# Kernel tuning notes

Hardware: AMD Instinct MI355X
Metric: run time of the kernel (lower is better)

The kernel has to match this reference:

```python
import jax, jax.numpy as jnp
import numpy as np

N = 50000      # num nodes
E = 800000     # num edges (avg degree 16)
H = 128        # hidden_dim
D = 3          # node_dim (decoder output)
L = 4          # num_layers


def setup_inputs() -> dict:
    key = jax.random.key(0)
    ks = jax.random.split(key, 6)
    s = 0.05
    x = jax.random.normal(ks[0], (N, H), dtype=jnp.float32)
    edge_index = jax.random.randint(ks[1], (2, E), 0, N, dtype=jnp.int64)
    # per-layer EdgeConv MLP params: Linear(2H->H), ReLU, Linear(H->H)
    W1 = jax.random.normal(ks[2], (L, 2 * H, H), dtype=jnp.float32) * s
    b1 = jnp.zeros((L, H), dtype=jnp.float32)
    W2 = jax.random.normal(ks[3], (L, H, H), dtype=jnp.float32) * s
    b2 = jnp.zeros((L, H), dtype=jnp.float32)
    # final fc: Linear(H -> D)
    Wf = jax.random.normal(ks[4], (H, D), dtype=jnp.float32) * s
    bf = jnp.zeros((D,), dtype=jnp.float32)
    return {"x": x, "edge_index": edge_index, "W1": W1, "b1": b1,
            "W2": W2, "b2": b2, "Wf": Wf, "bf": bf}


def reference(x, edge_index, W1, b1, W2, b2, Wf, bf):
    n = x.shape[0]
    # add_self_loops: every node has at least one incoming message
    loops = jnp.arange(n, dtype=edge_index.dtype)
    src = jnp.concatenate([edge_index[0], loops])  # x_j source
    dst = jnp.concatenate([edge_index[1], loops])  # x_i target / aggregate index
    for l in range(W1.shape[0]):
        x_i = x[dst]                                   # [E+N, H] gather targets
        x_j = x[src]                                   # [E+N, H] gather sources
        msg = jnp.concatenate([x_i, x_j - x_i], axis=-1)   # [E+N, 2H]
        msg = jax.nn.relu(msg @ W1[l] + b1[l]) @ W2[l] + b2[l]  # edge MLP
        x = jax.ops.segment_max(msg, dst, num_segments=n)       # max aggregate
    return x @ Wf + bf  # [N, D]
```

## Files before the change

kernel.cpp:

```cpp
#include <hip/hip_runtime.h>
#include <hip/hip_fp16.h>

typedef _Float16 f16;
typedef _Float16 f16x8 __attribute__((ext_vector_type(8)));
typedef __fp16 hf16x2 __attribute__((ext_vector_type(2)));
typedef float f32x4 __attribute__((ext_vector_type(4)));
typedef float f32x2 __attribute__((ext_vector_type(2)));
typedef unsigned int u32;
typedef u32 u32x4 __attribute__((ext_vector_type(4)));

#define HDIM 128
#define LAYERS 4
#define TS 32
#define NEG_BIG (-3.0e38f)

static __device__ __forceinline__ f32x4 mfma16(f16x8 a, f16x8 b, f32x4 c) {
  return __builtin_amdgcn_mfma_f32_16x16x32_f16(a, b, c, 0, 0, 0);
}

static __device__ __forceinline__ void atomicMaxF(float* addr, float val) {
  if (val >= 0.f) atomicMax((int*)addr, __float_as_int(val));
  else            atomicMin((unsigned int*)addr, __float_as_uint(val));
}

static __device__ __forceinline__ f16x8 pack4(hf16x2 a, hf16x2 b, hf16x2 c, hf16x2 d) {
  u32x4 u = {__builtin_bit_cast(u32, a), __builtin_bit_cast(u32, b),
             __builtin_bit_cast(u32, c), __builtin_bit_cast(u32, d)};
  return __builtin_bit_cast(f16x8, u);
}

static __device__ __forceinline__ void split8(f32x4 a, f32x4 b, f16x8& hv, f16x8& lv) {
  hf16x2 h0 = __builtin_amdgcn_cvt_pkrtz(a.x, a.y);
  hf16x2 h1 = __builtin_amdgcn_cvt_pkrtz(a.z, a.w);
  hf16x2 h2 = __builtin_amdgcn_cvt_pkrtz(b.x, b.y);
  hf16x2 h3 = __builtin_amdgcn_cvt_pkrtz(b.z, b.w);
  hv = pack4(h0, h1, h2, h3);
  hf16x2 l0 = __builtin_amdgcn_cvt_pkrtz(a.x - (float)h0[0], a.y - (float)h0[1]);
  hf16x2 l1 = __builtin_amdgcn_cvt_pkrtz(a.z - (float)h1[0], a.w - (float)h1[1]);
  hf16x2 l2 = __builtin_amdgcn_cvt_pkrtz(b.x - (float)h2[0], b.y - (float)h2[1]);
  hf16x2 l3 = __builtin_amdgcn_cvt_pkrtz(b.z - (float)h3[0], b.w - (float)h3[1]);
  lv = pack4(l0, l1, l2, l3);
}

__global__ void gnn_hist(const int* __restrict__ ei, int* __restrict__ deg, int E) {
  int e = blockIdx.x * 256 + threadIdx.x;
  if (e < E) atomicAdd(&deg[ei[E + e]], 1);
}

__global__ void gnn_bsum(const int* __restrict__ deg, int* __restrict__ bsum, int N) {
  __shared__ int red[256];
  int v = blockIdx.x * 256 + threadIdx.x;
  red[threadIdx.x] = (v < N) ? (deg[v] + 1) : 0;
  __syncthreads();
  for (int d = 128; d; d >>= 1) {
    if (threadIdx.x < d) red[threadIdx.x] += red[threadIdx.x + d];
    __syncthreads();
  }
  if (threadIdx.x == 0) bsum[blockIdx.x] = red[0];
}

__global__ void gnn_bscan(const int* __restrict__ bsum, int* __restrict__ boffs,
                          int* __restrict__ offs, int nb, int N) {
  __shared__ int sh[256];
  int t = threadIdx.x;
  sh[t] = (t < nb) ? bsum[t] : 0;
  __syncthreads();
  for (int d = 1; d < 256; d <<= 1) {
    int add = (t >= d) ? sh[t - d] : 0;
    __syncthreads();
    sh[t] += add;
    __syncthreads();
  }
  boffs[t] = (t > 0) ? sh[t - 1] : 0;
  if (t == 255) offs[N] = sh[255];
}

__global__ void gnn_scan_fin(const int* __restrict__ deg, const int* __restrict__ boffs,
                             int* __restrict__ offs, int* __restrict__ cursor,
                             int* __restrict__ colsrc, int* __restrict__ nodeof, int N) {
  __shared__ int sh[256];
  int t = threadIdx.x;
  int v = blockIdx.x * 256 + t;
  int val = (v < N) ? (deg[v] + 1) : 0;
  sh[t] = val;
  __syncthreads();
  for (int d = 1; d < 256; d <<= 1) {
    int add = (t >= d) ? sh[t - d] : 0;
    __syncthreads();
    sh[t] += add;
    __syncthreads();
  }
  if (v < N) {
    int excl = boffs[blockIdx.x] + sh[t] - val;
    offs[v] = excl;
    cursor[v] = excl + 1;
    colsrc[excl] = v;
    nodeof[excl] = v;
  }
}

__global__ void gnn_scatter(const int* __restrict__ ei, int* __restrict__ cursor,
                            int* __restrict__ colsrc, int* __restrict__ nodeof, int E) {
  int e = blockIdx.x * 256 + threadIdx.x;
  if (e < E) {
    int d = ei[E + e];
    int p = atomicAdd(&cursor[d], 1);
    colsrc[p] = ei[e];
    nodeof[p] = d;
  }
}

__global__ void gnn_biasprep(const float* __restrict__ W1, const float* __restrict__ b1,
                             const float* __restrict__ b2, const float* __restrict__ Wf,
                             const float* __restrict__ bf, float* __restrict__ cbias,
                             float* __restrict__ bfp) {
  int l = blockIdx.x, c = threadIdx.x;
  if (l < LAYERS) {
    float s = 0.f;
    if (l > 0) {
      const float* bp = b2 + (size_t)(l - 1) * HDIM;
      if (c < 128) {
        for (int k = 0; k < 128; k++)
          s += bp[k] * (W1[((size_t)l * 256 + k) * 128 + c] - W1[((size_t)l * 256 + 128 + k) * 128 + c]);
      } else {
        int cc = c - 128;
        for (int k = 0; k < 128; k++)
          s += bp[k] * W1[((size_t)l * 256 + 128 + k) * 128 + cc];
      }
    }
    float base = (c < 128) ? b1[(size_t)l * HDIM + c] : 0.f;
    cbias[l * 256 + c] = base + s;
  } else if (c < 3) {
    float s = bf[c];
    for (int k = 0; k < 128; k++) s += b2[3 * HDIM + k] * Wf[k * 3 + c];
    bfp[c] = s;
  }
}

__global__ void gnn_wprep1(const float* __restrict__ W1, f16* __restrict__ Wc) {
  int id = blockIdx.x * 256 + threadIdx.x;
  if (id >= LAYERS * 128 * 256) return;
  int col = id & 255, k = (id >> 8) & 127, l = id >> 15;
  float w;
  if (col < 128) w = W1[((size_t)l * 256 + k) * 128 + col] - W1[((size_t)l * 256 + 128 + k) * 128 + col];
  else           w = W1[((size_t)l * 256 + 128 + k) * 128 + (col - 128)];
  f16 hi = (f16)w;
  f16 lo = (f16)(w - (float)hi);
  int kk = k >> 5, quad = (k >> 3) & 3, j = k & 7;
  int ntile = col >> 4, lane = quad * 16 + (col & 15);
  size_t base = ((((size_t)l * 2 + 0) * 4 + kk) * 16 + ntile) * 512 + lane * 8 + j;
  Wc[base] = hi;
  Wc[base + (size_t)4 * 16 * 512] = lo;
}

__global__ void gnn_wprep2(const float* __restrict__ W2, f16* __restrict__ W2f) {
  int id = blockIdx.x * 256 + threadIdx.x;
  if (id >= LAYERS * 128 * 128) return;
  int n = id & 127, k = (id >> 7) & 127, l = id >> 14;
  float w = W2[((size_t)l * 128 + k) * 128 + n];
  f16 hi = (f16)w;
  f16 lo = (f16)(w - (float)hi);
  int kk = k >> 5, quad = (k >> 3) & 3, j = k & 7;
  int ntile = n >> 4, lane = quad * 16 + (n & 15);
  size_t base = ((((size_t)l * 2 + 0) * 4 + kk) * 8 + ntile) * 512 + lane * 8 + j;
  W2f[base] = hi;
  W2f[base + (size_t)4 * 8 * 512] = lo;
}

__global__ __launch_bounds__(256) void gnn_pq(const float* __restrict__ x,
    const f16* __restrict__ Wc, const float* __restrict__ cbias,
    float* __restrict__ P, float* __restrict__ Q, int N,
    const int* __restrict__ offs, int spb, float* __restrict__ xinit) {
  __shared__ __align__(16) f16 shA[2 * 4 * 4 * 64 * 8];
  int tid = threadIdx.x;
  int row0 = blockIdx.x * 64;
#pragma unroll
  for (int i = 0; i < 4; i++) {
    int p = i * 256 + tid;
    int row = p & 63, seg = p >> 6;
    f32x4 a = {}, b = {};
    int gr = row0 + row;
    if (gr < N) {
      const f32x4* xp = (const f32x4*)(x + (size_t)gr * HDIM + seg * 8);
      a = xp[0]; b = xp[1];
    }
    f16x8 hv, lv;
    split8(a, b, hv, lv);
    int kk = seg >> 2, quad = seg & 3, mt = row >> 4, m = row & 15;
    int lane = quad * 16 + m;
    int off = ((kk * 4 + mt) * 64 + lane) * 8;
    *(f16x8*)&shA[off] = hv;
    *(f16x8*)&shA[off + 4 * 4 * 64 * 8] = lv;
  }
  __syncthreads();
  int wave = tid >> 6, lane = tid & 63;
  int quad = lane >> 4, cl = lane & 15;
  f16x8 bw[2][4][4];
#pragma unroll
  for (int pl = 0; pl < 2; pl++)
#pragma unroll
    for (int nt = 0; nt < 4; nt++)
#pragma unroll
      for (int kk = 0; kk < 4; kk++) {
        int ntile = wave * 4 + nt;
        bw[pl][nt][kk] = *(const f16x8*)&Wc[(((size_t)(pl * 4 + kk) * 16 + ntile) * 64 + lane) * 8];
      }
#pragma unroll
  for (int mt = 0; mt < 4; mt++) {
    f32x4 acc[4] = {};
#pragma unroll
    for (int kk = 0; kk < 4; kk++) {
      f16x8 ah = *(const f16x8*)&shA[((kk * 4 + mt) * 64 + lane) * 8];
      f16x8 al = *(const f16x8*)&shA[(((4 + kk) * 4 + mt) * 64 + lane) * 8];
#pragma unroll
      for (int nt = 0; nt < 4; nt++) {
        acc[nt] = mfma16(ah, bw[0][nt][kk], acc[nt]);
        acc[nt] = mfma16(al, bw[0][nt][kk], acc[nt]);
        acc[nt] = mfma16(ah, bw[1][nt][kk], acc[nt]);
      }
    }
#pragma unroll
    for (int nt = 0; nt < 4; nt++) {
      int c = (wave * 4 + nt) * 16 + cl;
      float bb = cbias[c];
      float* dst = (c < HDIM) ? P : Q;
      int cc = c & 127;
#pragma unroll
      for (int i = 0; i < 4; i++) {
        int gr = row0 + mt * 16 + quad * 4 + i;
        if (gr < N) dst[(size_t)gr * HDIM + cc] = acc[nt][i] + bb;
      }
    }
  }
  if (tid < 64) {
    int v = row0 + tid;
    if (v < N) {
      int a = offs[v], b = offs[v + 1] - 1;
      if (a / spb != b / spb) {
        f32x4 ninf = {NEG_BIG, NEG_BIG, NEG_BIG, NEG_BIG};
        float* xr = xinit + (size_t)v * HDIM;
#pragma unroll
        for (int c = 0; c < HDIM; c += 4) *(f32x4*)(xr + c) = ninf;
      }
    }
  }
}

__global__ __launch_bounds__(256, 4) void gnn_edge8(
    const float* __restrict__ P, const float* __restrict__ Q,
    const int* __restrict__ offs, const int* __restrict__ colsrc,
    const int* __restrict__ nodeof, const f16* __restrict__ W2f,
    float* __restrict__ xout, int S, int spb) {
  __shared__ __align__(16) f16 shA[2 * 4 * 2 * 64 * 8];
  __shared__ __align__(16) float stradV[2][128];
  __shared__ int stradN[2];
  int tid = threadIdx.x;
  int wave = tid >> 6, lane = tid & 63;
  int quad = lane >> 4, cl = lane & 15;
  f16x8 bw[2][2][4];
#pragma unroll
  for (int pl = 0; pl < 2; pl++)
#pragma unroll
    for (int nt = 0; nt < 2; nt++)
#pragma unroll
      for (int kk = 0; kk < 4; kk++)
        bw[pl][nt][kk] = *(const f16x8*)&W2f[(((size_t)(pl * 4 + kk) * 8 + (wave * 2 + nt)) * 64 + lane) * 8];
  int blk0 = blockIdx.x * spb;
  int blk1 = blk0 + spb; if (blk1 > S) blk1 = S;
  if (tid < 2) stradN[tid] = -1;
  __syncthreads();
  int sl = tid >> 4, seg = tid & 15;
  int kkb = seg >> 2, qb = seg & 3;
  int laneF = qb * 16 + sl;
  int Sm1 = S - 1;
  int tc = 0;
  for (int t0 = blk0; t0 < blk1; t0 += TS, tc++) {
    int par = tc & 1, prv = par ^ 1;
    int tEnd = t0 + TS; if (tEnd > blk1) tEnd = blk1;
#pragma unroll
    for (int i = 0; i < 2; i++) {
      int slot = t0 + i * 16 + sl;
      int slc = (slot < S) ? slot : Sm1;
      int src = colsrc[slc];
      int dst = nodeof[slc];
      const f32x4* qp = (const f32x4*)(Q + (size_t)src * HDIM + seg * 8);
      const f32x4* pp = (const f32x4*)(P + (size_t)dst * HDIM + seg * 8);
      f32x4 qa = qp[0], qb4 = qp[1], pa = pp[0], pb = pp[1];
      f32x4 sa, sb;
      sa.x = fmaxf(pa.x + qa.x, 0.f); sa.y = fmaxf(pa.y + qa.y, 0.f);
      sa.z = fmaxf(pa.z + qa.z, 0.f); sa.w = fmaxf(pa.w + qa.w, 0.f);
      sb.x = fmaxf(pb.x + qb4.x, 0.f); sb.y = fmaxf(pb.y + qb4.y, 0.f);
      sb.z = fmaxf(pb.z + qb4.z, 0.f); sb.w = fmaxf(pb.w + qb4.w, 0.f);
      f16x8 hv, lv;
      split8(sa, sb, hv, lv);
      int off = ((kkb * 2 + i) * 64 + laneF) * 8;
      *(f16x8*)&shA[off] = hv;
      *(f16x8*)&shA[off + 4096] = lv;
    }
    __syncthreads();
    f32x4 acc[2][2] = {};
#pragma unroll
    for (int kk = 0; kk < 4; kk++)
#pragma unroll
      for (int mt = 0; mt < 2; mt++) {
        int off = ((kk * 2 + mt) * 64 + lane) * 8;
        f16x8 ah = *(const f16x8*)&shA[off];
        f16x8 al = *(const f16x8*)&shA[off + 4096];
#pragma unroll
        for (int nt = 0; nt < 2; nt++) {
          acc[mt][nt] = mfma16(ah, bw[0][nt][kk], acc[mt][nt]);
          acc[mt][nt] = mfma16(al, bw[0][nt][kk], acc[mt][nt]);
          acc[mt][nt] = mfma16(ah, bw[1][nt][kk], acc[mt][nt]);
        }
      }
    __syncthreads();
    int vA = nodeof[t0];
    int vB = nodeof[tEnd - 1];
    int sNp = stradN[prv];
    for (int v = vA; v <= vB; v++) {
      int a = offs[v], b = offs[v + 1];
      int r0 = (a > t0 ? a : t0) - t0;
      int r1 = (b < tEnd ? b : tEnd) - t0;
      float m0 = NEG_BIG, m1 = NEG_BIG;
#pragma unroll
      for (int mt = 0; mt < 2; mt++)
#pragma unroll
        for (int i = 0; i < 4; i++) {
          int row = mt * 16 + quad * 4 + i;
          bool in = (row >= r0) && (row < r1);
          m0 = fmaxf(m0, in ? acc[mt][0][i] : NEG_BIG);
          m1 = fmaxf(m1, in ? acc[mt][1][i] : NEG_BIG);
        }
      m0 = fmaxf(m0, __shfl_xor(m0, 16, 64));
      m0 = fmaxf(m0, __shfl_xor(m0, 32, 64));
      m1 = fmaxf(m1, __shfl_xor(m1, 16, 64));
      m1 = fmaxf(m1, __shfl_xor(m1, 32, 64));
      if (quad == 0) {
        int col0 = wave * 32 + cl, col1 = col0 + 16;
        if (v == sNp) {
          m0 = fmaxf(m0, stradV[prv][col0]);
          m1 = fmaxf(m1, stradV[prv][col1]);
        }
        bool carry = (b > tEnd) && (tEnd < blk1);
        if (carry) {
          stradV[par][col0] = m0;
          stradV[par][col1] = m1;
        } else {
          float* dp = &xout[(size_t)v * HDIM];
          if (a < blk0 || b > blk1) {
            atomicMaxF(dp + col0, m0);
            atomicMaxF(dp + col1, m1);
          } else {
            dp[col0] = m0;
            dp[col1] = m1;
          }
        }
        if (wave == 0 && cl == 0 && v == vB) stradN[par] = carry ? v : -1;
      }
    }
  }
}

__global__ __launch_bounds__(256) void gnn_fc(const float* __restrict__ x,
    const float* __restrict__ Wf, const float* __restrict__ bfp,
    float* __restrict__ out, int N) {
  int wave = threadIdx.x >> 6, lane = threadIdx.x & 63;
  int wid = blockIdx.x * 4 + wave, nw = gridDim.x * 4;
  int k0 = lane * 2;
  float w00 = Wf[k0 * 3 + 0], w01 = Wf[k0 * 3 + 1], w02 = Wf[k0 * 3 + 2];
  float w10 = Wf[k0 * 3 + 3], w11 = Wf[k0 * 3 + 4], w12 = Wf[k0 * 3 + 5];
  float bf0 = bfp[0], bf1 = bfp[1], bf2 = bfp[2];
  for (int v = wid; v < N; v += nw) {
    f32x2 xx = *(const f32x2*)(x + (size_t)v * HDIM + k0);
    float d0 = xx.x * w00 + xx.y * w10;
    float d1 = xx.x * w01 + xx.y * w11;
    float d2 = xx.x * w02 + xx.y * w12;
#pragma unroll
    for (int s = 32; s; s >>= 1) {
      d0 += __shfl_xor(d0, s, 64);
      d1 += __shfl_xor(d1, s, 64);
      d2 += __shfl_xor(d2, s, 64);
    }
    if (lane == 0) {
      out[(size_t)v * 3 + 0] = d0 + bf0;
      out[(size_t)v * 3 + 1] = d1 + bf1;
      out[(size_t)v * 3 + 2] = d2 + bf2;
    }
  }
}

extern "C" void kernel_launch(void* const* d_in, const int* in_sizes, int n_in,
                              void* d_out, int out_size, void* d_ws, size_t ws_size,
                              hipStream_t stream) {
  const float* x_in = (const float*)d_in[0];
  const int*   ei   = (const int*)d_in[1];
  const float* W1   = (const float*)d_in[2];
  const float* b1   = (const float*)d_in[3];
  const float* W2   = (const float*)d_in[4];
  const float* b2   = (const float*)d_in[5];
  const float* Wf   = (const float*)d_in[6];
  const float* bfv  = (const float*)d_in[7];
  float* outp = (float*)d_out;
  int N = in_sizes[0] / HDIM;
  int E = in_sizes[1] / 2;
  int S = E + N;

  char* ws = (char*)d_ws;
  size_t o = 0;
  auto alloc = [&](size_t bytes) -> char* {
    char* p = ws + o;
    o += (bytes + 255) & ~(size_t)255;
    return p;
  };
  int*   deg    = (int*)alloc((size_t)N * 4);
  int*   offs   = (int*)alloc(((size_t)N + 1) * 4);
  int*   cursor = (int*)alloc((size_t)N * 4);
  int*   colsrc = (int*)alloc((size_t)S * 4);
  int*   nodeof = (int*)alloc((size_t)S * 4);
  int*   bsum   = (int*)alloc(256 * 4);
  int*   boffs  = (int*)alloc(256 * 4);
  float* cbias  = (float*)alloc((size_t)LAYERS * 256 * 4);
  float* bfp    = (float*)alloc(4 * 4);
  float* P      = (float*)alloc((size_t)N * HDIM * 4);
  float* Q      = (float*)alloc((size_t)N * HDIM * 4);
  float* xbuf   = (float*)alloc((size_t)N * HDIM * 4);
  f16*   Wc     = (f16*)alloc((size_t)LAYERS * 65536 * 2);
  f16*   W2f    = (f16*)alloc((size_t)LAYERS * 32768 * 2);
  (void)ws_size; (void)n_in; (void)out_size;

  int nb = (N + 255) / 256;
  hipMemsetAsync(deg, 0, (size_t)N * 4, stream);
  gnn_hist<<<(E + 255) / 256, 256, 0, stream>>>(ei, deg, E);
  gnn_bsum<<<nb, 256, 0, stream>>>(deg, bsum, N);
  gnn_bscan<<<1, 256, 0, stream>>>(bsum, boffs, offs, nb, N);
  gnn_scan_fin<<<nb, 256, 0, stream>>>(deg, boffs, offs, cursor, colsrc, nodeof, N);
  gnn_scatter<<<(E + 255) / 256, 256, 0, stream>>>(ei, cursor, colsrc, nodeof, E);
  gnn_biasprep<<<LAYERS + 1, 256, 0, stream>>>(W1, b1, b2, Wf, bfv, cbias, bfp);
  gnn_wprep1<<<(LAYERS * 128 * 256 + 255) / 256, 256, 0, stream>>>(W1, Wc);
  gnn_wprep2<<<(LAYERS * 128 * 128 + 255) / 256, 256, 0, stream>>>(W2, W2f);

  int spb = ((((S + 2047) / 2048) + TS - 1) / TS) * TS;
  int NB = (S + spb - 1) / spb;
  const float* xc = x_in;
  for (int l = 0; l < LAYERS; l++) {
    gnn_pq<<<(N + 63) / 64, 256, 0, stream>>>(xc, Wc + (size_t)l * 65536, cbias + l * 256,
                                              P, Q, N, offs, spb, xbuf);
    gnn_edge8<<<NB, 256, 0, stream>>>(P, Q, offs, colsrc, nodeof, W2f + (size_t)l * 32768,
                                      xbuf, S, spb);
    xc = xbuf;
  }
  gnn_fc<<<256, 256, 0, stream>>>(xc, Wf, bfp, outp, N);
}
```

Before: 841.1 us.

## Software-pipeline edge gathers with double-buffered LDS tiles in edge kernel

Restructures the edge kernel so the P/Q row gathers and index loads for the next 32-edge tile are issued before the current tile's MFMA and max-reduction work, using a double-buffered shared-memory A tile. This removes one barrier per tile and is meant to hide global gather latency behind compute. In exchange it holds more live registers, so launch bounds drop from 4 to 3 blocks per SIMD-occupancy hint, which may reduce occupancy-based latency hiding.

```diff
diff --git a/kernel.cpp b/kernel.cpp
--- a/kernel.cpp
+++ b/kernel.cpp
@@ -246,12 +246,12 @@
   }
 }
 
-__global__ __launch_bounds__(256, 4) void gnn_edge8(
+__global__ __launch_bounds__(256, 3) void gnn_edge10(
     const float* __restrict__ P, const float* __restrict__ Q,
     const int* __restrict__ offs, const int* __restrict__ colsrc,
     const int* __restrict__ nodeof, const f16* __restrict__ W2f,
     float* __restrict__ xout, int S, int spb) {
-  __shared__ __align__(16) f16 shA[2 * 4 * 2 * 64 * 8];
+  __shared__ __align__(16) f16 shA[2][8192];
   __shared__ __align__(16) float stradV[2][128];
   __shared__ int stradN[2];
   int tid = threadIdx.x;
@@ -268,44 +268,72 @@
   int blk0 = blockIdx.x * spb;
   int blk1 = blk0 + spb; if (blk1 > S) blk1 = S;
   if (tid < 2) stradN[tid] = -1;
-  __syncthreads();
   int sl = tid >> 4, seg = tid & 15;
   int kkb = seg >> 2, qb = seg & 3;
   int laneF = qb * 16 + sl;
   int Sm1 = S - 1;
+
+  int cs[2], nd[2];
+  f32x4 qv[2][2], pv[2][2];
+#pragma unroll
+  for (int i = 0; i < 2; i++) {
+    int slc = blk0 + i * 16 + sl; slc = (slc < S) ? slc : Sm1;
+    cs[i] = colsrc[slc]; nd[i] = nodeof[slc];
+  }
+#pragma unroll
+  for (int i = 0; i < 2; i++) {
+    const f32x4* qp = (const f32x4*)(Q + (size_t)cs[i] * HDIM + seg * 8);
+    const f32x4* pp = (const f32x4*)(P + (size_t)nd[i] * HDIM + seg * 8);
+    qv[i][0] = qp[0]; qv[i][1] = qp[1];
+    pv[i][0] = pp[0]; pv[i][1] = pp[1];
+  }
+#pragma unroll
+  for (int i = 0; i < 2; i++) {
+    int slc = blk0 + TS + i * 16 + sl; slc = (slc < S) ? slc : Sm1;
+    cs[i] = colsrc[slc]; nd[i] = nodeof[slc];
+  }
+#pragma unroll
+  for (int i = 0; i < 2; i++) {
+    f32x4 sa, sb;
+    sa.x = fmaxf(pv[i][0].x + qv[i][0].x, 0.f); sa.y = fmaxf(pv[i][0].y + qv[i][0].y, 0.f);
+    sa.z = fmaxf(pv[i][0].z + qv[i][0].z, 0.f); sa.w = fmaxf(pv[i][0].w + qv[i][0].w, 0.f);
+    sb.x = fmaxf(pv[i][1].x + qv[i][1].x, 0.f); sb.y = fmaxf(pv[i][1].y + qv[i][1].y, 0.f);
+    sb.z = fmaxf(pv[i][1].z + qv[i][1].z, 0.f); sb.w = fmaxf(pv[i][1].w + qv[i][1].w, 0.f);
+    f16x8 hv, lv;
+    split8(sa, sb, hv, lv);
+    int off = ((kkb * 2 + i) * 64 + laneF) * 8;
+    *(f16x8*)&shA[0][off] = hv;
+    *(f16x8*)&shA[0][off + 4096] = lv;
+  }
+  __syncthreads();
+
   int tc = 0;
   for (int t0 = blk0; t0 < blk1; t0 += TS, tc++) {
     int par = tc & 1, prv = par ^ 1;
     int tEnd = t0 + TS; if (tEnd > blk1) tEnd = blk1;
-#pragma unroll
-    for (int i = 0; i < 2; i++) {
-      int slot = t0 + i * 16 + sl;
-      int slc = (slot < S) ? slot : Sm1;
-      int src = colsrc[slc];
-      int dst = nodeof[slc];
-      const f32x4* qp = (const f32x4*)(Q + (size_t)src * HDIM + seg * 8);
-      const f32x4* pp = (const f32x4*)(P + (size_t)dst * HDIM + seg * 8);
-      f32x4 qa = qp[0], qb4 = qp[1], pa = pp[0], pb = pp[1];
-      f32x4 sa, sb;
-      sa.x = fmaxf(pa.x + qa.x, 0.f); sa.y = fmaxf(pa.y + qa.y, 0.f);
-      sa.z = fmaxf(pa.z + qa.z, 0.f); sa.w = fmaxf(pa.w + qa.w, 0.f);
-      sb.x = fmaxf(pb.x + qb4.x, 0.f); sb.y = fmaxf(pb.y + qb4.y, 0.f);
-      sb.z = fmaxf(pb.z + qb4.z, 0.f); sb.w = fmaxf(pb.w + qb4.w, 0.f);
-      f16x8 hv, lv;
-      split8(sa, sb, hv, lv);
-      int off = ((kkb * 2 + i) * 64 + laneF) * 8;
-      *(f16x8*)&shA[off] = hv;
-      *(f16x8*)&shA[off + 4096] = lv;
-    }
-    __syncthreads();
+    bool hasNext = (t0 + TS) < blk1;
+    if (hasNext) {
+#pragma unroll
+      for (int i = 0; i < 2; i++) {
+        const f32x4* qp = (const f32x4*)(Q + (size_t)cs[i] * HDIM + seg * 8);
+        const f32x4* pp = (const f32x4*)(P + (size_t)nd[i] * HDIM + seg * 8);
+        qv[i][0] = qp[0]; qv[i][1] = qp[1];
+        pv[i][0] = pp[0]; pv[i][1] = pp[1];
+      }
+#pragma unroll
+      for (int i = 0; i < 2; i++) {
+        int slc = t0 + 2 * TS + i * 16 + sl; slc = (slc < S) ? slc : Sm1;
+        cs[i] = colsrc[slc]; nd[i] = nodeof[slc];
+      }
+    }
     f32x4 acc[2][2] = {};
 #pragma unroll
     for (int kk = 0; kk < 4; kk++)
 #pragma unroll
       for (int mt = 0; mt < 2; mt++) {
         int off = ((kk * 2 + mt) * 64 + lane) * 8;
-        f16x8 ah = *(const f16x8*)&shA[off];
-        f16x8 al = *(const f16x8*)&shA[off + 4096];
+        f16x8 ah = *(const f16x8*)&shA[par][off];
+        f16x8 al = *(const f16x8*)&shA[par][off + 4096];
 #pragma unroll
         for (int nt = 0; nt < 2; nt++) {
           acc[mt][nt] = mfma16(ah, bw[0][nt][kk], acc[mt][nt]);
@@ -313,7 +341,6 @@
           acc[mt][nt] = mfma16(ah, bw[1][nt][kk], acc[mt][nt]);
         }
       }
-    __syncthreads();
     int vA = nodeof[t0];
     int vB = nodeof[tEnd - 1];
     int sNp = stradN[prv];
@@ -358,6 +385,22 @@
         if (wave == 0 && cl == 0 && v == vB) stradN[par] = carry ? v : -1;
       }
     }
+    if (hasNext) {
+#pragma unroll
+      for (int i = 0; i < 2; i++) {
+        f32x4 sa, sb;
+        sa.x = fmaxf(pv[i][0].x + qv[i][0].x, 0.f); sa.y = fmaxf(pv[i][0].y + qv[i][0].y, 0.f);
+        sa.z = fmaxf(pv[i][0].z + qv[i][0].z, 0.f); sa.w = fmaxf(pv[i][0].w + qv[i][0].w, 0.f);
+        sb.x = fmaxf(pv[i][1].x + qv[i][1].x, 0.f); sb.y = fmaxf(pv[i][1].y + qv[i][1].y, 0.f);
+        sb.z = fmaxf(pv[i][1].z + qv[i][1].z, 0.f); sb.w = fmaxf(pv[i][1].w + qv[i][1].w, 0.f);
+        f16x8 hv, lv;
+        split8(sa, sb, hv, lv);
+        int off = ((kkb * 2 + i) * 64 + laneF) * 8;
+        *(f16x8*)&shA[par ^ 1][off] = hv;
+        *(f16x8*)&shA[par ^ 1][off + 4096] = lv;
+      }
+    }
+    __syncthreads();
   }
 }
 
@@ -445,8 +488,8 @@
   for (int l = 0; l < LAYERS; l++) {
     gnn_pq<<<(N + 63) / 64, 256, 0, stream>>>(xc, Wc + (size_t)l * 65536, cbias + l * 256,
                                               P, Q, N, offs, spb, xbuf);
-    gnn_edge8<<<NB, 256, 0, stream>>>(P, Q, offs, colsrc, nodeof, W2f + (size_t)l * 32768,
-                                      xbuf, S, spb);
+    gnn_edge10<<<NB, 256, 0, stream>>>(P, Q, offs, colsrc, nodeof, W2f + (size_t)l * 32768,
+                                       xbuf, S, spb);
     xc = xbuf;
   }
   gnn_fc<<<256, 256, 0, stream>>>(xc, Wf, bfp, outp, N);
```

Measured after the change: 887.2 us. 1.05x slower.
